# Kernel optimization log

Hardware: AMD Instinct MI355X
Metric: run time of the kernel (lower is better)

Reference implementation:

```python
import jax, jax.numpy as jnp
import numpy as np

N, E, D, C = 10000, 320000, 128, 3  # nodes, edges, hidden/feat dim, coord dim


def _lin_init(key, fan_in, fan_out, bias=True):
    k1, k2 = jax.random.split(key)
    bound = 1.0 / np.sqrt(fan_in)
    W = jax.random.uniform(k1, (fan_in, fan_out), jnp.float32, -bound, bound)
    if bias:
        b = jax.random.uniform(k2, (fan_out,), jnp.float32, -bound, bound)
        return W, b
    return W


def setup_inputs() -> dict:
    key = jax.random.key(0)
    ks = jax.random.split(key, 12)
    h = jax.random.normal(ks[0], (N, D), jnp.float32)
    coord = jax.random.normal(ks[1], (N, C), jnp.float32)
    edge_index = jax.random.randint(ks[2], (2, E), 0, N, jnp.int64)
    We1, be1 = _lin_init(ks[3], 2 * D + 1, D)   # edge_mlp layer 1
    We2, be2 = _lin_init(ks[4], D, D)           # edge_mlp layer 2
    Wa, ba = _lin_init(ks[5], D, 1)             # att_mlp
    Wn1, bn1 = _lin_init(ks[6], D + D, D)       # node_mlp layer 1
    Wn2, bn2 = _lin_init(ks[7], D, D)           # node_mlp layer 2
    Wc1, bc1 = _lin_init(ks[8], D, D)           # coord_mlp layer 1
    Wc2 = _lin_init(ks[9], D, 1, bias=False)    # coord_mlp layer 2 (no bias)
    return dict(h=h, edge_index=edge_index, coord=coord,
                We1=We1, be1=be1, We2=We2, be2=be2, Wa=Wa, ba=ba,
                Wn1=Wn1, bn1=bn1, Wn2=Wn2, bn2=bn2, Wc1=Wc1, bc1=bc1, Wc2=Wc2)


def reference(h, edge_index, coord, We1, be1, We2, be2, Wa, ba,
              Wn1, bn1, Wn2, bn2, Wc1, bc1, Wc2):
    row, col = edge_index[0], edge_index[1]
    # coord2radial (normalize=False)
    coord_diff = coord[row] - coord[col]                      # [E, 3]
    radial = jnp.sum(coord_diff ** 2, axis=1, keepdims=True)  # [E, 1]
    # edge_model: cat(source, target, radial) -> MLP -> attention gate
    e_in = jnp.concatenate([h[row], h[col], radial], axis=1)  # [E, 2D+1]
    m = jax.nn.silu(e_in @ We1 + be1)
    m = jax.nn.silu(m @ We2 + be2)                            # [E, D]
    att = jax.nn.sigmoid(m @ Wa + ba)                         # [E, 1]
    edge_feat = m * att                                       # [E, D]
    # coord_model: scatter-mean of gated coord diffs
    w = jax.nn.silu(edge_feat @ Wc1 + bc1) @ Wc2              # [E, 1]
    trans = coord_diff * w                                    # [E, 3]
    agg_c = jax.ops.segment_sum(trans, row, num_segments=N)
    cnt = jax.ops.segment_sum(jnp.ones((E,), jnp.float32), row, num_segments=N)
    coord_out = coord + agg_c / jnp.maximum(cnt, 1.0)[:, None]
    # node_model: scatter-sum of edge features, residual MLP
    agg_h = jax.ops.segment_sum(edge_feat, row, num_segments=N)  # [N, D]
    n_in = jnp.concatenate([h, agg_h], axis=1)
    out = jax.nn.silu(n_in @ Wn1 + bn1) @ Wn2 + bn2
    h_out = h + out  # residual=True
    return h_out, coord_out
```

## Files before the change

kernel.cpp:

```cpp
#include <hip/hip_runtime.h>
#include <hip/hip_bf16.h>

#define NN 10000
#define EE 320000
#define DD 128
#define TEE 128

typedef __attribute__((ext_vector_type(8))) __bf16 bf16x8;
typedef __attribute__((ext_vector_type(2))) __bf16 bf16x2;
typedef __attribute__((ext_vector_type(8))) unsigned short ushort8;
typedef __attribute__((ext_vector_type(4))) float  f32x4;

__device__ __forceinline__ float silu_f(float x) {
    return x * __builtin_amdgcn_rcpf(1.0f + __expf(-x));
}
__device__ __forceinline__ float sigmoid_f(float x) {
    return __builtin_amdgcn_rcpf(1.0f + __expf(-x));
}
__device__ __forceinline__ unsigned pkbf(float a, float b) {
    bf16x2 v; v.x = (__bf16)a; v.y = (__bf16)b;
    return __builtin_bit_cast(unsigned, v);
}
__device__ __forceinline__ unsigned short sbf(float a) {
    return __builtin_bit_cast(unsigned short, (__bf16)a);
}
__device__ __forceinline__ float bf2f(unsigned short u) {
    return __builtin_bit_cast(float, (unsigned)u << 16);
}
__device__ __forceinline__ float atomic_add_f(float* p, float v) {
    return unsafeAtomicAdd(p, v);
}

__global__ __launch_bounds__(256)
void front_kernel(const int* __restrict__ ei, int* __restrict__ cnt,
                  const float* __restrict__ We1, const float* __restrict__ We2,
                  const float* __restrict__ Wc1, const float* __restrict__ Wn1,
                  const float* __restrict__ Wn2, unsigned short* __restrict__ pW,
                  float* __restrict__ aggz)
{
    const int b = blockIdx.x;
    const int tid = threadIdx.x;
    if (b < 313) {
        const int t4 = b * 256 + tid;
        if (t4 < EE / 4) {
            const int4 e4 = *(const int4*)&ei[t4 * 4];
            atomicAdd(&cnt[e4.x], 1);
            atomicAdd(&cnt[e4.y], 1);
            atomicAdd(&cnt[e4.z], 1);
            atomicAdd(&cnt[e4.w], 1);
        }
    } else if (b < 761) {
        const int idx = (b - 313) * 256 + tid;
        const float* src; int loc, nks, koff = 0;
        if (idx < 16384)       { src = We1; loc = idx;         nks = 4; }
        else if (idx < 32768)  { src = We1; loc = idx - 16384; nks = 4; koff = 128; }
        else if (idx < 49152)  { src = We2; loc = idx - 32768; nks = 4; }
        else if (idx < 65536)  { src = Wc1; loc = idx - 49152; nks = 4; }
        else if (idx < 98304)  { src = Wn1; loc = idx - 65536; nks = 8; }
        else                   { src = Wn2; loc = idx - 98304; nks = 4; }
        const int per_ct = nks * 512;
        const int ct = loc / per_ct;
        const int r  = loc % per_ct;
        const int ks = r >> 9;
        const int r2 = r & 511;
        const int ln = r2 >> 3;
        const int j  = r2 & 7;
        const int k  = ks * 32 + (ln >> 4) * 8 + j + koff;
        const int n  = ct * 16 + (ln & 15);
        pW[idx] = sbf(src[k * DD + n]);
    } else {
        const int base = ((b - 761) * 256 + tid) * 4;
        float4* p = (float4*)aggz;
#pragma unroll
        for (int k = 0; k < 4; ++k) {
            const int i = base + k;
            if (i < 327500) p[i] = make_float4(0.f, 0.f, 0.f, 0.f);
        }
    }
}

__global__ __launch_bounds__(256)
void alloc_kernel(const int* __restrict__ cnt, int* __restrict__ offs,
                  int* __restrict__ ctr)
{
    const int n = blockIdx.x * 256 + threadIdx.x;
    if (n < NN) offs[n] = atomicAdd(ctr, cnt[n]);
}

__global__ __launch_bounds__(256, 2)
void mid_kernel(const int* __restrict__ ei, const int* __restrict__ offs,
                int* __restrict__ tmp, int2* __restrict__ eidx,
                const float* __restrict__ h, const float* __restrict__ be1,
                const unsigned short* __restrict__ pW,
                unsigned short* __restrict__ P, unsigned short* __restrict__ Q)
{
    const int b = blockIdx.x;
    const int tid = threadIdx.x;
    if (b < 1250) {
        const int e = b * 256 + tid;
        if (e < EE) {
            const int r = ei[e];
            const int c = ei[EE + e];
            const int pos = offs[r] + atomicAdd(&tmp[r], 1);
            eidx[pos] = make_int2(r, c);
        }
        return;
    }
    __shared__ __align__(16) unsigned short sAbuf[32 * 128];
    const int w    = tid >> 6;
    const int lane = tid & 63;
    const int g    = lane >> 4;
    const int l15  = lane & 15;
    const int n0   = (b - 1250) * 32;
    char* const sAb = (char*)sAbuf;

#pragma unroll
    for (int i = 0; i < 2; ++i) {
        const int idx = tid * 2 + i;
        const int row = idx >> 4, c = idx & 15;
        const int n = n0 + row;
        float4 a = make_float4(0.f, 0.f, 0.f, 0.f);
        float4 bb = make_float4(0.f, 0.f, 0.f, 0.f);
        if (n < NN) {
            a  = *(const float4*)&h[(size_t)n * DD + c * 8];
            bb = *(const float4*)&h[(size_t)n * DD + c * 8 + 4];
        }
        uint4 pk;
        pk.x = pkbf(a.x, a.y);  pk.y = pkbf(a.z, a.w);
        pk.z = pkbf(bb.x, bb.y); pk.w = pkbf(bb.z, bb.w);
        *(uint4*)(sAb + row * 256 + ((c * 16) ^ ((row & 7) << 4))) = pk;
    }
    __syncthreads();

    f32x4 accP[2][2], accQ[2][2];
    {
        float be1c[2];
#pragma unroll
        for (int ctl = 0; ctl < 2; ++ctl)
            be1c[ctl] = be1[w * 32 + ctl * 16 + l15];
#pragma unroll
        for (int rt = 0; rt < 2; ++rt)
#pragma unroll
            for (int ctl = 0; ctl < 2; ++ctl)
#pragma unroll
                for (int j = 0; j < 4; ++j) {
                    accP[rt][ctl][j] = be1c[ctl];
                    accQ[rt][ctl][j] = 0.f;
                }
    }
    const unsigned short* pWa = pW;
    const unsigned short* pWb = pW + 16384;
#pragma unroll 1
    for (int ks = 0; ks < 4; ++ks) {
        bf16x8 a[2];
#pragma unroll
        for (int rt = 0; rt < 2; ++rt) {
            const int row = rt * 16 + l15;
            const int byc = g * 16 + ks * 64;
            a[rt] = *(const bf16x8*)(sAb + row * 256 + (byc ^ ((row & 7) << 4)));
        }
        const bf16x8 pa0 = *(const bf16x8*)&pWa[(((2 * w + 0) * 4 + ks) * 64 + lane) * 8];
        const bf16x8 pa1 = *(const bf16x8*)&pWa[(((2 * w + 1) * 4 + ks) * 64 + lane) * 8];
        const bf16x8 pb0 = *(const bf16x8*)&pWb[(((2 * w + 0) * 4 + ks) * 64 + lane) * 8];
        const bf16x8 pb1 = *(const bf16x8*)&pWb[(((2 * w + 1) * 4 + ks) * 64 + lane) * 8];
#pragma unroll
        for (int rt = 0; rt < 2; ++rt) {
            accP[rt][0] = __builtin_amdgcn_mfma_f32_16x16x32_bf16(a[rt], pa0, accP[rt][0], 0, 0, 0);
            accP[rt][1] = __builtin_amdgcn_mfma_f32_16x16x32_bf16(a[rt], pa1, accP[rt][1], 0, 0, 0);
            accQ[rt][0] = __builtin_amdgcn_mfma_f32_16x16x32_bf16(a[rt], pb0, accQ[rt][0], 0, 0, 0);
            accQ[rt][1] = __builtin_amdgcn_mfma_f32_16x16x32_bf16(a[rt], pb1, accQ[rt][1], 0, 0, 0);
        }
    }
#pragma unroll
    for (int rt = 0; rt < 2; ++rt)
#pragma unroll
        for (int ctl = 0; ctl < 2; ++ctl)
#pragma unroll
            for (int j = 0; j < 4; ++j) {
                const int row = rt * 16 + g * 4 + j;
                const int n = n0 + row;
                if (n < NN) {
                    const int col = w * 32 + ctl * 16 + l15;
                    P[(size_t)n * DD + col] = sbf(accP[rt][ctl][j]);
                    Q[(size_t)n * DD + col] = sbf(accQ[rt][ctl][j]);
                }
            }
}

__global__ __launch_bounds__(512, 6)
void edge_kernel(const int2* __restrict__ eidx,
                 const float* __restrict__ coord,
                 const unsigned short* __restrict__ P, const unsigned short* __restrict__ Q,
                 const float* __restrict__ We1,
                 const float* __restrict__ be2,
                 const float* __restrict__ Wa, const float* __restrict__ ba,
                 const float* __restrict__ bc1, const float* __restrict__ Wc2,
                 const unsigned short* __restrict__ pW,
                 float* __restrict__ agg_h, float* __restrict__ agg_c)
{
    __shared__ __align__(16) unsigned short sM[128 * 128];
    __shared__ __align__(16) float sWred[4][128];
    __shared__ __align__(16) int   sRow[128];
    __shared__ int   sCol[128];
    __shared__ __align__(16) float sRad[128];
    __shared__ __align__(16) float sAtt[128];
    __shared__ float sCd[128][3];

    const int tid  = threadIdx.x;
    const int w    = tid >> 6;
    const int lane = tid & 63;
    const int g    = lane >> 4;
    const int l15  = lane & 15;
    const int rh   = w >> 2;
    const int cq   = w & 3;
    const int rb   = rh * 64;
    const int e0g  = blockIdx.x * TEE;
    char* const sMb = (char*)sM;

    if (tid < TEE) {
        const int2 rc = eidx[e0g + tid];
        sRow[tid] = rc.x; sCol[tid] = rc.y;
        const float dx = coord[rc.x * 3 + 0] - coord[rc.y * 3 + 0];
        const float dy = coord[rc.x * 3 + 1] - coord[rc.y * 3 + 1];
        const float dz = coord[rc.x * 3 + 2] - coord[rc.y * 3 + 2];
        sCd[tid][0] = dx; sCd[tid][1] = dy; sCd[tid][2] = dz;
        sRad[tid] = dx * dx + dy * dy + dz * dz;
    }
    __syncthreads();

    {
        const int el  = tid >> 2;
        const int sub = tid & 3;
        const int rg = sRow[el], cg = sCol[el];
        const float rad = sRad[el];
        const unsigned short* Prow = P + (size_t)rg * DD;
        const unsigned short* Qrow = Q + (size_t)cg * DD;
        const float* We1r = We1 + 256 * DD;
#pragma unroll
        for (int i = 0; i < 4; ++i) {
            const int c8 = sub * 4 + i;
            const ushort8 pu = __builtin_bit_cast(ushort8, *(const bf16x8*)&Prow[c8 * 8]);
            const ushort8 qu = __builtin_bit_cast(ushort8, *(const bf16x8*)&Qrow[c8 * 8]);
            const float4 w0 = *(const float4*)&We1r[c8 * 8];
            const float4 w1 = *(const float4*)&We1r[c8 * 8 + 4];
            float x[8];
            x[0] = fmaf(rad, w0.x, bf2f(pu[0]) + bf2f(qu[0]));
            x[1] = fmaf(rad, w0.y, bf2f(pu[1]) + bf2f(qu[1]));
            x[2] = fmaf(rad, w0.z, bf2f(pu[2]) + bf2f(qu[2]));
            x[3] = fmaf(rad, w0.w, bf2f(pu[3]) + bf2f(qu[3]));
            x[4] = fmaf(rad, w1.x, bf2f(pu[4]) + bf2f(qu[4]));
            x[5] = fmaf(rad, w1.y, bf2f(pu[5]) + bf2f(qu[5]));
            x[6] = fmaf(rad, w1.z, bf2f(pu[6]) + bf2f(qu[6]));
            x[7] = fmaf(rad, w1.w, bf2f(pu[7]) + bf2f(qu[7]));
            uint4 pk;
            pk.x = pkbf(silu_f(x[0]), silu_f(x[1]));
            pk.y = pkbf(silu_f(x[2]), silu_f(x[3]));
            pk.z = pkbf(silu_f(x[4]), silu_f(x[5]));
            pk.w = pkbf(silu_f(x[6]), silu_f(x[7]));
            *(uint4*)(sMb + el * 256 + ((c8 * 16) ^ ((el & 7) << 4))) = pk;
        }
    }
    __syncthreads();

    f32x4 acc[4][2];

    {
        float be2c[2];
#pragma unroll
        for (int ctl = 0; ctl < 2; ++ctl)
            be2c[ctl] = be2[cq * 32 + ctl * 16 + l15];
#pragma unroll
        for (int rt = 0; rt < 4; ++rt)
#pragma unroll
            for (int ctl = 0; ctl < 2; ++ctl)
#pragma unroll
                for (int j = 0; j < 4; ++j)
                    acc[rt][ctl][j] = be2c[ctl];
        const unsigned short* pWe2 = pW + 32768;
#pragma unroll 1
        for (int ks = 0; ks < 4; ++ks) {
            bf16x8 a[4];
#pragma unroll
            for (int rt = 0; rt < 4; ++rt) {
                const int row = rb + rt * 16 + l15;
                const int byc = g * 16 + ks * 64;
                a[rt] = *(const bf16x8*)(sMb + row * 256 + (byc ^ ((row & 7) << 4)));
            }
            const bf16x8 b0 = *(const bf16x8*)&pWe2[(((2 * cq + 0) * 4 + ks) * 64 + lane) * 8];
            const bf16x8 b1 = *(const bf16x8*)&pWe2[(((2 * cq + 1) * 4 + ks) * 64 + lane) * 8];
#pragma unroll
            for (int rt = 0; rt < 4; ++rt) {
                acc[rt][0] = __builtin_amdgcn_mfma_f32_16x16x32_bf16(a[rt], b0, acc[rt][0], 0, 0, 0);
                acc[rt][1] = __builtin_amdgcn_mfma_f32_16x16x32_bf16(a[rt], b1, acc[rt][1], 0, 0, 0);
            }
        }
    }
#pragma unroll
    for (int rt = 0; rt < 4; ++rt)
#pragma unroll
        for (int ctl = 0; ctl < 2; ++ctl)
#pragma unroll
            for (int j = 0; j < 4; ++j)
                acc[rt][ctl][j] = silu_f(acc[rt][ctl][j]);

    {
        float wac[2];
#pragma unroll
        for (int ctl = 0; ctl < 2; ++ctl)
            wac[ctl] = Wa[cq * 32 + ctl * 16 + l15];
        float part[4][4];
#pragma unroll
        for (int rt = 0; rt < 4; ++rt)
#pragma unroll
            for (int j = 0; j < 4; ++j)
                part[rt][j] = fmaf(acc[rt][0][j], wac[0], acc[rt][1][j] * wac[1]);
#pragma unroll
        for (int msk = 1; msk < 16; msk <<= 1)
#pragma unroll
            for (int rt = 0; rt < 4; ++rt)
#pragma unroll
                for (int j = 0; j < 4; ++j)
                    part[rt][j] += __shfl_xor(part[rt][j], msk);
        if (l15 == 0) {
#pragma unroll
            for (int rt = 0; rt < 4; ++rt) {
                float4 p4 = make_float4(part[rt][0], part[rt][1], part[rt][2], part[rt][3]);
                *(float4*)&sWred[cq][rb + rt * 16 + g * 4] = p4;
            }
        }
    }
    __syncthreads();

#pragma unroll
    for (int rt = 0; rt < 4; ++rt)
#pragma unroll
        for (int ctl = 0; ctl < 2; ++ctl)
#pragma unroll
            for (int j = 0; j < 4; ++j) {
                const int row = rb + rt * 16 + g * 4 + j;
                const int col = cq * 32 + ctl * 16 + l15;
                *(unsigned short*)(sMb + row * 256 + ((col * 2) ^ ((row & 7) << 4)))
                    = sbf(acc[rt][ctl][j]);
            }
    if (tid < TEE) {
        const float s = sWred[0][tid] + sWred[1][tid] + sWred[2][tid] + sWred[3][tid];
        sAtt[tid] = sigmoid_f(s + ba[0]);
    }
    __syncthreads();

    {
        float bc1c[2];
#pragma unroll
        for (int ctl = 0; ctl < 2; ++ctl)
            bc1c[ctl] = bc1[cq * 32 + ctl * 16 + l15];
#pragma unroll
        for (int rt = 0; rt < 4; ++rt)
#pragma unroll
            for (int ctl = 0; ctl < 2; ++ctl)
#pragma unroll
                for (int j = 0; j < 4; ++j)
                    acc[rt][ctl][j] = 0.f;
        const unsigned short* pWc1 = pW + 49152;
#pragma unroll 1
        for (int ks = 0; ks < 4; ++ks) {
            bf16x8 a[4];
#pragma unroll
            for (int rt = 0; rt < 4; ++rt) {
                const int row = rb + rt * 16 + l15;
                const int byc = g * 16 + ks * 64;
                a[rt] = *(const bf16x8*)(sMb + row * 256 + (byc ^ ((row & 7) << 4)));
            }
            const bf16x8 b0 = *(const bf16x8*)&pWc1[(((2 * cq + 0) * 4 + ks) * 64 + lane) * 8];
            const bf16x8 b1 = *(const bf16x8*)&pWc1[(((2 * cq + 1) * 4 + ks) * 64 + lane) * 8];
#pragma unroll
            for (int rt = 0; rt < 4; ++rt) {
                acc[rt][0] = __builtin_amdgcn_mfma_f32_16x16x32_bf16(a[rt], b0, acc[rt][0], 0, 0, 0);
                acc[rt][1] = __builtin_amdgcn_mfma_f32_16x16x32_bf16(a[rt], b1, acc[rt][1], 0, 0, 0);
            }
        }
        float wcc[2];
#pragma unroll
        for (int ctl = 0; ctl < 2; ++ctl)
            wcc[ctl] = Wc2[cq * 32 + ctl * 16 + l15];
        float part[4][4];
#pragma unroll
        for (int rt = 0; rt < 4; ++rt) {
            const float4 a4 = *(const float4*)&sAtt[rb + rt * 16 + g * 4];
            const float at[4] = {a4.x, a4.y, a4.z, a4.w};
#pragma unroll
            for (int j = 0; j < 4; ++j) {
                const float z0 = silu_f(fmaf(at[j], acc[rt][0][j], bc1c[0]));
                const float z1 = silu_f(fmaf(at[j], acc[rt][1][j], bc1c[1]));
                part[rt][j] = fmaf(z0, wcc[0], z1 * wcc[1]);
            }
        }
#pragma unroll
        for (int msk = 1; msk < 16; msk <<= 1)
#pragma unroll
            for (int rt = 0; rt < 4; ++rt)
#pragma unroll
                for (int j = 0; j < 4; ++j)
                    part[rt][j] += __shfl_xor(part[rt][j], msk);
        if (l15 == 0) {
#pragma unroll
            for (int rt = 0; rt < 4; ++rt) {
                float4 p4 = make_float4(part[rt][0], part[rt][1], part[rt][2], part[rt][3]);
                *(float4*)&sWred[cq][rb + rt * 16 + g * 4] = p4;
            }
        }
    }
    __syncthreads();

    {
        const int col = tid & 127;
        const int seg = tid >> 7;
        const int ebeg = seg * 32;
        float a = 0.f;
        int cur = sRow[ebeg];
#pragma unroll 1
        for (int e = ebeg; e < ebeg + 32; ++e) {
            const int r = sRow[e];
            if (r != cur) {
                atomic_add_f(&agg_h[(size_t)cur * DD + col], a);
                a = 0.f; cur = r;
            }
            const unsigned short u =
                *(const unsigned short*)(sMb + e * 256 + ((col * 2) ^ ((e & 7) << 4)));
            a = fmaf(sAtt[e], bf2f(u), a);
        }
        atomic_add_f(&agg_h[(size_t)cur * DD + col], a);
    }

    if (tid < 12) {
        const int c = tid % 3;
        const int seg = tid / 3;
        const int ebeg = seg * 32;
        float a = 0.f;
        int cur = sRow[ebeg];
#pragma unroll 1
        for (int e = ebeg; e < ebeg + 32; ++e) {
            const int r = sRow[e];
            if (r != cur) {
                atomic_add_f(&agg_c[cur * 3 + c], a);
                a = 0.f; cur = r;
            }
            const float wv = sWred[0][e] + sWred[1][e] + sWred[2][e] + sWred[3][e];
            a += sCd[e][c] * wv;
        }
        atomic_add_f(&agg_c[cur * 3 + c], a);
    }
}

__global__ __launch_bounds__(256, 2)
void node_kernel(const float* __restrict__ h, const float* __restrict__ coord,
                 const float* __restrict__ bn1, const float* __restrict__ bn2,
                 const unsigned short* __restrict__ pW,
                 const float* __restrict__ agg_h, const float* __restrict__ agg_c,
                 const int* __restrict__ cnt,
                 float* __restrict__ hout, float* __restrict__ cout)
{
    __shared__ __align__(16) unsigned short sAbuf[32 * 256];

    const int tid  = threadIdx.x;
    const int w    = tid >> 6;
    const int lane = tid & 63;
    const int g    = lane >> 4;
    const int l15  = lane & 15;
    const int n0   = blockIdx.x * 32;
    char* const sAb = (char*)sAbuf;

    {
        const int halfsel = (lane >= 32) ? 1 : 0;
        const int bytec   = (lane & 31) * 8 + halfsel * 256;
        const float* src  = halfsel ? agg_h : h;
#pragma unroll 4
        for (int s = 0; s < 8; ++s) {
            const int row = w * 8 + s;
            const int n = n0 + row;
            float4 v = make_float4(0.f, 0.f, 0.f, 0.f);
            if (n < NN) v = *(const float4*)&src[(size_t)n * DD + (lane & 31) * 4];
            uint2 pk;
            pk.x = pkbf(v.x, v.y);
            pk.y = pkbf(v.z, v.w);
            *(uint2*)(sAb + row * 512 + (bytec ^ ((row & 7) << 4))) = pk;
        }
    }
    __syncthreads();

    f32x4 acc[2][2];

    {
        float bc[2];
#pragma unroll
        for (int ctl = 0; ctl < 2; ++ctl)
            bc[ctl] = bn1[w * 32 + ctl * 16 + l15];
#pragma unroll
        for (int rt = 0; rt < 2; ++rt)
#pragma unroll
            for (int ctl = 0; ctl < 2; ++ctl)
#pragma unroll
                for (int j = 0; j < 4; ++j)
                    acc[rt][ctl][j] = bc[ctl];
        const unsigned short* pWn1 = pW + 65536;
#pragma unroll 1
        for (int ks = 0; ks < 8; ++ks) {
            bf16x8 a[2];
#pragma unroll
            for (int rt = 0; rt < 2; ++rt) {
                const int row = rt * 16 + l15;
                const int byc = g * 16 + ks * 64;
                a[rt] = *(const bf16x8*)(sAb + row * 512 + (byc ^ ((row & 7) << 4)));
            }
            const bf16x8 b0 = *(const bf16x8*)&pWn1[(((2 * w + 0) * 8 + ks) * 64 + lane) * 8];
            const bf16x8 b1 = *(const bf16x8*)&pWn1[(((2 * w + 1) * 8 + ks) * 64 + lane) * 8];
#pragma unroll
            for (int rt = 0; rt < 2; ++rt) {
                acc[rt][0] = __builtin_amdgcn_mfma_f32_16x16x32_bf16(a[rt], b0, acc[rt][0], 0, 0, 0);
                acc[rt][1] = __builtin_amdgcn_mfma_f32_16x16x32_bf16(a[rt], b1, acc[rt][1], 0, 0, 0);
            }
        }
    }
    __syncthreads();
#pragma unroll
    for (int rt = 0; rt < 2; ++rt)
#pragma unroll
        for (int ctl = 0; ctl < 2; ++ctl)
#pragma unroll
            for (int j = 0; j < 4; ++j) {
                const int row = rt * 16 + g * 4 + j;
                const int col = w * 32 + ctl * 16 + l15;
                *(unsigned short*)(sAb + row * 256 + ((col * 2) ^ ((row & 7) << 4)))
                    = sbf(silu_f(acc[rt][ctl][j]));
            }
    __syncthreads();

    {
        float bc[2];
#pragma unroll
        for (int ctl = 0; ctl < 2; ++ctl)
            bc[ctl] = bn2[w * 32 + ctl * 16 + l15];
#pragma unroll
        for (int rt = 0; rt < 2; ++rt)
#pragma unroll
            for (int ctl = 0; ctl < 2; ++ctl)
#pragma unroll
                for (int j = 0; j < 4; ++j)
                    acc[rt][ctl][j] = bc[ctl];
        const unsigned short* pWn2 = pW + 98304;
#pragma unroll 1
        for (int ks = 0; ks < 4; ++ks) {
            bf16x8 a[2];
#pragma unroll
            for (int rt = 0; rt < 2; ++rt) {
                const int row = rt * 16 + l15;
                const int byc = g * 16 + ks * 64;
                a[rt] = *(const bf16x8*)(sAb + row * 256 + (byc ^ ((row & 7) << 4)));
            }
            const bf16x8 b0 = *(const bf16x8*)&pWn2[(((2 * w + 0) * 4 + ks) * 64 + lane) * 8];
            const bf16x8 b1 = *(const bf16x8*)&pWn2[(((2 * w + 1) * 4 + ks) * 64 + lane) * 8];
#pragma unroll
            for (int rt = 0; rt < 2; ++rt) {
                acc[rt][0] = __builtin_amdgcn_mfma_f32_16x16x32_bf16(a[rt], b0, acc[rt][0], 0, 0, 0);
                acc[rt][1] = __builtin_amdgcn_mfma_f32_16x16x32_bf16(a[rt], b1, acc[rt][1], 0, 0, 0);
            }
        }
    }
#pragma unroll
    for (int rt = 0; rt < 2; ++rt)
#pragma unroll
        for (int ctl = 0; ctl < 2; ++ctl)
#pragma unroll
            for (int j = 0; j < 4; ++j) {
                const int row = rt * 16 + g * 4 + j;
                const int n = n0 + row;
                if (n < NN) {
                    const int col = w * 32 + ctl * 16 + l15;
                    hout[(size_t)n * DD + col] = h[(size_t)n * DD + col] + acc[rt][ctl][j];
                }
            }

    if (tid < 96) {
        const int e = tid / 3, c = tid % 3;
        const int n = n0 + e;
        if (n < NN) {
            const float cn = fmaxf((float)cnt[n], 1.0f);
            cout[n * 3 + c] = coord[n * 3 + c] + agg_c[n * 3 + c] / cn;
        }
    }
}

extern "C" void kernel_launch(void* const* d_in, const int* in_sizes, int n_in,
                              void* d_out, int out_size, void* d_ws, size_t ws_size,
                              hipStream_t stream)
{
    const float* h     = (const float*)d_in[0];
    const int*   ei    = (const int*)  d_in[1];
    const float* coord = (const float*)d_in[2];
    const float* We1   = (const float*)d_in[3];
    const float* be1   = (const float*)d_in[4];
    const float* We2   = (const float*)d_in[5];
    const float* be2   = (const float*)d_in[6];
    const float* Wa    = (const float*)d_in[7];
    const float* ba    = (const float*)d_in[8];
    const float* Wn1   = (const float*)d_in[9];
    const float* bn1   = (const float*)d_in[10];
    const float* Wn2   = (const float*)d_in[11];
    const float* bn2   = (const float*)d_in[12];
    const float* Wc1   = (const float*)d_in[13];
    const float* bc1   = (const float*)d_in[14];
    const float* Wc2   = (const float*)d_in[15];

    float* agg_h   = (float*)d_ws;
    float* agg_c   = agg_h + (size_t)NN * DD;
    int*   cnt_i   = (int*)(agg_c + (size_t)NN * 3);
    int*   tmp_i   = cnt_i + NN;
    int*   offs    = tmp_i + NN;
    int2*  eidx    = (int2*)(offs + 10016);
    unsigned short* pW = (unsigned short*)(eidx + EE);
    unsigned short* P  = pW + 114688;
    unsigned short* Q  = P + (size_t)NN * DD;
    int* ctr = offs + 10008;

    (void)hipMemsetAsync(cnt_i, 0, (size_t)(2 * NN + 10016) * sizeof(int), stream);

    front_kernel<<<1081, 256, 0, stream>>>(ei, cnt_i, We1, We2, Wc1, Wn1, Wn2,
                                           pW, agg_h);
    alloc_kernel<<<40, 256, 0, stream>>>(cnt_i, offs, ctr);
    mid_kernel<<<1563, 256, 0, stream>>>(ei, offs, tmp_i, eidx, h, be1, pW, P, Q);

    edge_kernel<<<EE / TEE, 512, 0, stream>>>(eidx, coord, P, Q, We1, be2,
                                              Wa, ba, bc1, Wc2, pW, agg_h, agg_c);

    float* hout = (float*)d_out;
    float* cout = hout + (size_t)NN * DD;
    node_kernel<<<313, 256, 0, stream>>>(h, coord, bn1, bn2, pW,
                                         agg_h, agg_c, cnt_i, hout, cout);
}
```

Baseline: 183.0 us.

## Merge memset, front, alloc and mid kernels into one cooperative kernel

Replaces the memset plus three preprocessing launches (degree counting, weight packing, offset allocation, CSR fill and node projection) with a single cooperative kernel. Stages are separated by grid.sync instead of kernel boundaries. The goal is to remove launch overheads and inter-kernel gaps. In exchange, the node-projection work now runs on only 313 blocks after the edge scatter, which removes the overlap it previously had with the scatter blocks. The 1024-block cooperative launch also requires at least four resident blocks per CU.

```diff
diff --git a/kernel.cpp b/kernel.cpp
--- a/kernel.cpp
+++ b/kernel.cpp
@@ -1,10 +1,14 @@
 #include <hip/hip_runtime.h>
 #include <hip/hip_bf16.h>
+#include <hip/hip_cooperative_groups.h>
+
+namespace cg = cooperative_groups;
 
 #define NN 10000
 #define EE 320000
 #define DD 128
 #define TEE 128
+#define COOPB 1024
 
 typedef __attribute__((ext_vector_type(8))) __bf16 bf16x8;
 typedef __attribute__((ext_vector_type(2))) __bf16 bf16x2;
@@ -31,26 +35,27 @@
     return unsafeAtomicAdd(p, v);
 }
 
-__global__ __launch_bounds__(256)
-void front_kernel(const int* __restrict__ ei, int* __restrict__ cnt,
-                  const float* __restrict__ We1, const float* __restrict__ We2,
-                  const float* __restrict__ Wc1, const float* __restrict__ Wn1,
-                  const float* __restrict__ Wn2, unsigned short* __restrict__ pW,
-                  float* __restrict__ aggz)
+__global__ __launch_bounds__(256, 4)
+void coop_kernel(const int* __restrict__ ei,
+                 int* __restrict__ cnt, int* __restrict__ tmp,
+                 int* __restrict__ offs, int* __restrict__ ctr,
+                 int2* __restrict__ eidx,
+                 const float* __restrict__ h, const float* __restrict__ be1,
+                 const float* __restrict__ We1, const float* __restrict__ We2,
+                 const float* __restrict__ Wc1, const float* __restrict__ Wn1,
+                 const float* __restrict__ Wn2,
+                 unsigned short* __restrict__ pW,
+                 unsigned short* __restrict__ P, unsigned short* __restrict__ Q,
+                 float* __restrict__ aggz)
 {
-    const int b = blockIdx.x;
-    const int tid = threadIdx.x;
-    if (b < 313) {
-        const int t4 = b * 256 + tid;
-        if (t4 < EE / 4) {
-            const int4 e4 = *(const int4*)&ei[t4 * 4];
-            atomicAdd(&cnt[e4.x], 1);
-            atomicAdd(&cnt[e4.y], 1);
-            atomicAdd(&cnt[e4.z], 1);
-            atomicAdd(&cnt[e4.w], 1);
-        }
-    } else if (b < 761) {
-        const int idx = (b - 313) * 256 + tid;
+    cg::grid_group grid = cg::this_grid();
+    const int b    = blockIdx.x;
+    const int tid  = threadIdx.x;
+    const int gtid = b * 256 + tid;
+    const int GT   = COOPB * 256;
+
+    if (gtid < 114688) {
+        const int idx = gtid;
         const float* src; int loc, nks, koff = 0;
         if (idx < 16384)       { src = We1; loc = idx;         nks = 4; }
         else if (idx < 32768)  { src = We1; loc = idx - 16384; nks = 4; koff = 128; }
@@ -68,50 +73,39 @@
         const int k  = ks * 32 + (ln >> 4) * 8 + j + koff;
         const int n  = ct * 16 + (ln & 15);
         pW[idx] = sbf(src[k * DD + n]);
-    } else {
-        const int base = ((b - 761) * 256 + tid) * 4;
+    } else if (gtid < 114688 + 2 * NN) {
+        cnt[gtid - 114688] = 0;
+    } else if (gtid == 114688 + 2 * NN) {
+        *ctr = 0;
+    }
+    {
         float4* p = (float4*)aggz;
-#pragma unroll
-        for (int k = 0; k < 4; ++k) {
-            const int i = base + k;
-            if (i < 327500) p[i] = make_float4(0.f, 0.f, 0.f, 0.f);
-        }
-    }
-}
-
-__global__ __launch_bounds__(256)
-void alloc_kernel(const int* __restrict__ cnt, int* __restrict__ offs,
-                  int* __restrict__ ctr)
-{
-    const int n = blockIdx.x * 256 + threadIdx.x;
-    if (n < NN) offs[n] = atomicAdd(ctr, cnt[n]);
-}
-
-__global__ __launch_bounds__(256, 2)
-void mid_kernel(const int* __restrict__ ei, const int* __restrict__ offs,
-                int* __restrict__ tmp, int2* __restrict__ eidx,
-                const float* __restrict__ h, const float* __restrict__ be1,
-                const unsigned short* __restrict__ pW,
-                unsigned short* __restrict__ P, unsigned short* __restrict__ Q)
-{
-    const int b = blockIdx.x;
-    const int tid = threadIdx.x;
-    if (b < 1250) {
-        const int e = b * 256 + tid;
-        if (e < EE) {
-            const int r = ei[e];
-            const int c = ei[EE + e];
-            const int pos = offs[r] + atomicAdd(&tmp[r], 1);
-            eidx[pos] = make_int2(r, c);
-        }
-        return;
-    }
+        for (int i = gtid; i < 327500; i += GT)
+            p[i] = make_float4(0.f, 0.f, 0.f, 0.f);
+    }
+    grid.sync();
+
+    for (int e = gtid; e < EE; e += GT)
+        atomicAdd(&cnt[ei[e]], 1);
+    grid.sync();
+
+    if (gtid < NN) offs[gtid] = atomicAdd(ctr, cnt[gtid]);
+    grid.sync();
+
+    for (int e = gtid; e < EE; e += GT) {
+        const int r = ei[e];
+        const int c = ei[EE + e];
+        const int pos = offs[r] + atomicAdd(&tmp[r], 1);
+        eidx[pos] = make_int2(r, c);
+    }
+
+    if (b >= 313) return;
     __shared__ __align__(16) unsigned short sAbuf[32 * 128];
     const int w    = tid >> 6;
     const int lane = tid & 63;
     const int g    = lane >> 4;
     const int l15  = lane & 15;
-    const int n0   = (b - 1250) * 32;
+    const int n0   = b * 32;
     char* const sAb = (char*)sAbuf;
 
 #pragma unroll
@@ -621,12 +615,16 @@
     unsigned short* Q  = P + (size_t)NN * DD;
     int* ctr = offs + 10008;
 
-    (void)hipMemsetAsync(cnt_i, 0, (size_t)(2 * NN + 10016) * sizeof(int), stream);
-
-    front_kernel<<<1081, 256, 0, stream>>>(ei, cnt_i, We1, We2, Wc1, Wn1, Wn2,
-                                           pW, agg_h);
-    alloc_kernel<<<40, 256, 0, stream>>>(cnt_i, offs, ctr);
-    mid_kernel<<<1563, 256, 0, stream>>>(ei, offs, tmp_i, eidx, h, be1, pW, P, Q);
+    {
+        void* args[] = {
+            (void*)&ei, (void*)&cnt_i, (void*)&tmp_i, (void*)&offs, (void*)&ctr,
+            (void*)&eidx, (void*)&h, (void*)&be1, (void*)&We1, (void*)&We2,
+            (void*)&Wc1, (void*)&Wn1, (void*)&Wn2, (void*)&pW,
+            (void*)&P, (void*)&Q, (void*)&agg_h
+        };
+        (void)hipLaunchCooperativeKernel((const void*)coop_kernel,
+                                         dim3(COOPB), dim3(256), args, 0, stream);
+    }
 
     edge_kernel<<<EE / TEE, 512, 0, stream>>>(eidx, coord, P, Q, We1, be2,
                                               Wa, ba, bc1, Wc2, pW, agg_h, agg_c);
```

New measurement: 458.6 us. 2.51x slower.
